# Kernel optimization log

Hardware: AMD Instinct MI355X
Metric: run time of the kernel (lower is better)

## Reference

```python
import jax, jax.numpy as jnp
import numpy as np

GROUP_SIZE = 128  # vLLM machete default group size
ZERO_POINT = 8.0  # uint4b8: stored unsigned 4-bit, logical value = q - 8


def setup_inputs() -> dict:
    key = jax.random.key(0)
    k_a, k_b, k_s = jax.random.split(key, 3)
    M, K, N = 4096, 4096, 12288
    a = jax.random.normal(k_a, (M, K), dtype=jnp.float32)
    # int4 quantized weights stored as small ints in [0, 16)
    b_q = jax.random.randint(k_b, (K, N), 0, 16, dtype=jnp.int32)
    # per-group scales: one scale per (group of 128 rows of K) per output column
    scales = jax.random.uniform(k_s, (K // GROUP_SIZE, N), dtype=jnp.float32) * 0.02 + 0.001
    return {"a": a, "b_q": b_q, "scales": scales}


def reference(a, b_q, scales):
    K, N = b_q.shape
    G = K // GROUP_SIZE
    # dequantize: (q - 8) * group_scale, scale broadcast over each K-group
    b = (b_q.astype(jnp.float32) - ZERO_POINT).reshape(G, GROUP_SIZE, N)
    b = (b * scales[:, None, :]).reshape(K, N)  # [K, N] dequantized weights
    return a @ b  # [M, N]
```

## Files before the change

kernel.cpp:

```cpp
#include <hip/hip_runtime.h>
#include <hip/hip_bf16.h>
#include <stdint.h>

constexpr int Mdim = 4096;
constexpr int Kdim = 4096;
constexpr int Ndim = 12288;

constexpr int NKT = Kdim / 64;
constexpr int GM256 = Mdim / 256;
constexpr int GN256 = Ndim / 256;
constexpr int NWG256 = GM256 * GN256;
constexpr int GRID_M = Mdim / 128;
constexpr int GRID_N = Ndim / 128;
constexpr int NWG = GRID_M * GRID_N;

typedef float  f32x4   __attribute__((ext_vector_type(4)));
typedef __bf16 bf16x4v __attribute__((ext_vector_type(4)));
typedef __bf16 bf16x8v __attribute__((ext_vector_type(8)));
typedef int    i32x4   __attribute__((ext_vector_type(4)));
typedef unsigned short ushort8 __attribute__((ext_vector_type(8)));

typedef __attribute__((address_space(3))) uint32_t       lds_u32;
typedef __attribute__((address_space(1))) const uint32_t glb_u32;

__device__ __forceinline__ void gload16(const void* g, void* l) {
    __builtin_amdgcn_global_load_lds((glb_u32*)(uintptr_t)g,
                                     (lds_u32*)(uint32_t)(uintptr_t)l, 16, 0, 0);
}


__launch_bounds__(256)
__global__ void cvtA(const float* __restrict__ A, unsigned short* __restrict__ Aw) {
    int t = blockIdx.x * 256 + threadIdx.x;
    int r = t >> 9;
    int c = t & 511;
    const float* src = A + ((long)r << 12) + (c << 3);
    f32x4 v0 = *(const f32x4*)src;
    f32x4 v1 = *(const f32x4*)(src + 4);
    bf16x8v o;
#pragma unroll
    for (int j = 0; j < 4; ++j) { o[j] = (__bf16)v0[j]; o[4 + j] = (__bf16)v1[j]; }
    int ks = c & 3;
    int cp = (c & ~3) | (ks ^ ((r >> 1) & 3));
    *(bf16x8v*)(Aw + ((long)r << 12) + (cp << 3)) = o;
}

__launch_bounds__(256)
__global__ void deqB(const int* __restrict__ Bq, const float* __restrict__ S,
                     unsigned short* __restrict__ Bw) {
    __shared__ unsigned short lt[64][72];
    int kb = blockIdx.x & 63;
    int nb = blockIdx.x >> 6;
    int k0 = kb << 6, n0 = nb << 6;
    int tid = threadIdx.x;
    int g = k0 >> 7;
    int nq = (tid & 15) << 2;
    f32x4 sc = *(const f32x4*)(S + (long)g * Ndim + n0 + nq);
#pragma unroll
    for (int p = 0; p < 4; ++p) {
        int kk = (p << 4) + (tid >> 4);
        i32x4 q = *(const i32x4*)(Bq + (long)(k0 + kk) * Ndim + n0 + nq);
#pragma unroll
        for (int j = 0; j < 4; ++j) {
            float v = ((float)q[j] - 8.f) * sc[j];
            lt[nq + j][kk] = __builtin_bit_cast(unsigned short, (__bf16)v);
        }
    }
    __syncthreads();
#pragma unroll
    for (int h = 0; h < 2; ++h) {
        int cidx = tid + (h << 8);
        int n = cidx >> 3, sidx = cidx & 7;
        int kh = sidx >> 2, ks = sidx & 3;
        int ksp = ks ^ ((n >> 1) & 3);
        ushort8 v = *(const ushort8*)&lt[n][sidx << 3];
        *(ushort8*)(Bw + (long)(n0 + n) * Kdim + k0 + kh * 32 + ksp * 8) = v;
    }
}

__launch_bounds__(512, 2)
__global__ void gemm256(const unsigned short* __restrict__ Aw,
                        const unsigned short* __restrict__ Bw,
                        float* __restrict__ C) {
    extern __shared__ unsigned char ldsbuf[];

    const int tid  = threadIdx.x;
    const int lane = tid & 63;
    const int w    = tid >> 6;
    const int wr   = w >> 2, wc = w & 3;
    const int fr   = lane & 15;
    const int ks   = lane >> 4;

    const int bid = blockIdx.x;
    const int xcd = bid & 7;
    const int loc = bid >> 3;
    const int pn  = loc >> 4;
    const int tm  = loc & 15;
    const int tn  = xcd * 6 + pn;
    const int brow = tm << 8, bcol = tn << 8;

    const unsigned char* pA = (const unsigned char*)Aw
        + (size_t)(brow + (tid >> 2)) * 8192 + (size_t)(tid & 3) * 16;
    const unsigned char* pA2 = pA + (size_t)128 * 8192;
    const unsigned char* pB = (const unsigned char*)Bw
        + (size_t)(bcol + (tid >> 2)) * 8192 + (size_t)(tid & 3) * 16;
    const unsigned char* pB2 = pB + (size_t)128 * 8192;
    const int ldw = w << 10;

    int offA[8][2], offB[4][2];
#pragma unroll
    for (int am = 0; am < 8; ++am)
#pragma unroll
        for (int kh = 0; kh < 2; ++kh) {
            int rowL = wr * 128 + am * 16 + fr;
            offA[am][kh] = (kh << 14) + rowL * 64 + ((ks ^ ((rowL >> 1) & 3)) << 4);
        }
#pragma unroll
    for (int n = 0; n < 4; ++n)
#pragma unroll
        for (int kh = 0; kh < 2; ++kh) {
            int colL = wc * 64 + n * 16 + fr;
            offB[n][kh] = (kh << 14) + colL * 64 + ((ks ^ ((colL >> 1) & 3)) << 4);
        }

    f32x4 acc[8][4];
#pragma unroll
    for (int m = 0; m < 8; ++m)
#pragma unroll
        for (int n = 0; n < 4; ++n) acc[m][n] = (f32x4){0.f, 0.f, 0.f, 0.f};

#define STG_A(DSTB, OFF)                                                      \
    gload16(pA  + (OFF), ldsbuf + (DSTB) + ldw);                              \
    gload16(pA2 + (OFF), ldsbuf + (DSTB) + ldw + 8192);
#define STG_B(DSTB, OFF)                                                      \
    gload16(pB  + (OFF), ldsbuf + (DSTB) + 32768 + ldw);                      \
    gload16(pB2 + (OFF), ldsbuf + (DSTB) + 32768 + ldw + 8192);

#define TILE(BUF, OFF, STG)                                                   \
    {                                                                         \
        unsigned char* sAc = ldsbuf + ((BUF) << 16);                          \
        unsigned char* sBc = sAc + 32768;                                     \
        bf16x8v a0[8], b0[4], a1[8], b1[4];                                   \
        _Pragma("unroll") for (int m = 0; m < 8; ++m)                         \
            a0[m] = *(const bf16x8v*)(sAc + offA[m][0]);                      \
        _Pragma("unroll") for (int n = 0; n < 4; ++n)                         \
            b0[n] = *(const bf16x8v*)(sBc + offB[n][0]);                      \
        if (STG) {                                                            \
            STG_A(((1 - (BUF)) << 16), OFF)                                   \
            STG_B(((1 - (BUF)) << 16), OFF)                                   \
            STG_A(((1 - (BUF)) << 16) + (1 << 14), (OFF) + 64)                \
            STG_B(((1 - (BUF)) << 16) + (1 << 14), (OFF) + 64)                \
        }                                                                     \
        __builtin_amdgcn_s_setprio(1);                                        \
        _Pragma("unroll") for (int m = 0; m < 8; ++m)                         \
            _Pragma("unroll") for (int n = 0; n < 4; ++n)                     \
                acc[m][n] = __builtin_amdgcn_mfma_f32_16x16x32_bf16(          \
                    a0[m], b0[n], acc[m][n], 0, 0, 0);                        \
        __builtin_amdgcn_s_setprio(0);                                        \
        _Pragma("unroll") for (int m = 0; m < 8; ++m)                         \
            a1[m] = *(const bf16x8v*)(sAc + offA[m][1]);                      \
        _Pragma("unroll") for (int n = 0; n < 4; ++n)                         \
            b1[n] = *(const bf16x8v*)(sBc + offB[n][1]);                      \
        __builtin_amdgcn_s_setprio(1);                                        \
        _Pragma("unroll") for (int m = 0; m < 8; ++m)                         \
            _Pragma("unroll") for (int n = 0; n < 4; ++n)                     \
                acc[m][n] = __builtin_amdgcn_mfma_f32_16x16x32_bf16(          \
                    a1[m], b1[n], acc[m][n], 0, 0, 0);                        \
        __builtin_amdgcn_s_setprio(0);                                        \
        asm volatile("s_waitcnt vmcnt(0)" ::: "memory");                      \
        __builtin_amdgcn_s_barrier();                                         \
    }

    STG_A(0, 0)          STG_B(0, 0)
    STG_A((1 << 14), 64) STG_B((1 << 14), 64)
    asm volatile("s_waitcnt vmcnt(0)" ::: "memory");
    __builtin_amdgcn_s_barrier();

    for (int it = 0; it < 31; ++it) {
        TILE(0, 128, 1)
        TILE(1, 256, 1)
        pA += 256; pA2 += 256; pB += 256; pB2 += 256;
    }
    TILE(0, 128, 1)
    TILE(1, 0, 0)

#pragma unroll
    for (int m = 0; m < 8; ++m) {
        int row = brow + wr * 128 + m * 16 + ks * 4;
#pragma unroll
        for (int n = 0; n < 4; ++n) {
            int col = bcol + wc * 64 + n * 16 + fr;
            f32x4 v = acc[m][n];
            float* cp = C + (size_t)row * Ndim + col;
#pragma unroll
            for (int r = 0; r < 4; ++r) cp[(size_t)r * Ndim] = v[r];
        }
    }
#undef TILE
#undef STG_B
#undef STG_A
}

__launch_bounds__(256, 3)
__global__ void gemm_bf16(const unsigned short* __restrict__ Aw,
                          const unsigned short* __restrict__ Bw,
                          float* __restrict__ C) {
    __shared__ unsigned char sA[128 * 64 * 2];
    __shared__ unsigned char sB[128 * 64 * 2];

    const int tid  = threadIdx.x;
    const int lane = tid & 63;
    const int w    = tid >> 6;

    const int bid   = blockIdx.x;
    const int x     = bid & 7;
    const int local = bid >> 3;
    const int pn    = local >> 5;
    const int tm    = local & 31;
    const int tn    = x * 12 + pn;
    const int brow  = tm << 7;
    const int bcol  = tn << 7;

    const unsigned char* ga[4];
    const unsigned char* gb[4];
#pragma unroll
    for (int i = 0; i < 4; ++i) {
        int c = (w << 8) + (i << 6) + lane;
        int r = c >> 3, s = c & 7;
        ga[i] = (const unsigned char*)Aw + (long)(brow + r) * 8192 + (s << 4);
        gb[i] = (const unsigned char*)Bw + (long)(bcol + r) * 8192 + (s << 4);
    }

    const int fr = lane & 15;
    const int ks = lane >> 4;
    const int wr = w >> 1, wc = w & 1;
    int ra[4][2], rb[4][2];
#pragma unroll
    for (int m = 0; m < 4; ++m)
#pragma unroll
        for (int kk = 0; kk < 2; ++kk) {
            int r_a = wr * 64 + m * 16 + fr;
            int r_b = wc * 64 + m * 16 + fr;
            ra[m][kk] = (r_a << 7) + (kk << 6) + ((ks ^ ((r_a >> 1) & 3)) << 4);
            rb[m][kk] = (r_b << 7) + (kk << 6) + ((ks ^ ((r_b >> 1) & 3)) << 4);
        }

    f32x4 acc[4][4];
#pragma unroll
    for (int m = 0; m < 4; ++m)
#pragma unroll
        for (int n = 0; n < 4; ++n) acc[m][n] = (f32x4){0.f, 0.f, 0.f, 0.f};

    for (int kt = 0; kt < NKT; ++kt) {
#pragma unroll
        for (int i = 0; i < 4; ++i) {
            gload16(ga[i], sA + (((w << 2) + i) << 10));
            gload16(gb[i], sB + (((w << 2) + i) << 10));
            ga[i] += 128;
            gb[i] += 128;
        }
        __syncthreads();

#pragma unroll
        for (int kk = 0; kk < 2; ++kk) {
            bf16x8v af[4], bf[4];
#pragma unroll
            for (int m = 0; m < 4; ++m) af[m] = *(const bf16x8v*)(sA + ra[m][kk]);
#pragma unroll
            for (int n = 0; n < 4; ++n) bf[n] = *(const bf16x8v*)(sB + rb[n][kk]);
#pragma unroll
            for (int m = 0; m < 4; ++m)
#pragma unroll
                for (int n = 0; n < 4; ++n)
                    acc[m][n] = __builtin_amdgcn_mfma_f32_16x16x32_bf16(af[m], bf[n], acc[m][n], 0, 0, 0);
        }
        __syncthreads();
    }

#pragma unroll
    for (int m = 0; m < 4; ++m) {
        int row = brow + wr * 64 + m * 16 + ks * 4;
#pragma unroll
        for (int n = 0; n < 4; ++n) {
            int col = bcol + wc * 64 + n * 16 + fr;
            f32x4 v = acc[m][n];
            float* cp = C + (long)row * Ndim + col;
#pragma unroll
            for (int r = 0; r < 4; ++r) cp[(long)r * Ndim] = v[r];
        }
    }
}

__device__ __forceinline__ int swz_f(int row, int kbyte) {
    int s = kbyte >> 4;
    int f = s ^ ((row ^ (row >> 2)) & 7);
    return (row << 7) + (f << 4) + (kbyte & 15);
}

__launch_bounds__(256, 2)
__global__ void machete_fused(const float* __restrict__ A,
                              const int* __restrict__ Bq,
                              const float* __restrict__ S,
                              float* __restrict__ C) {
    __shared__ unsigned char sA[128 * 64 * 2];
    __shared__ unsigned char sB[128 * 64 * 2];

    const int tid = threadIdx.x;
    const int bid = blockIdx.x;
    const int sid = (bid & 7) * (NWG / 8) + (bid >> 3);
    const int tm = sid / GRID_N;
    const int tn = sid % GRID_N;
    const int brow = tm * 128;
    const int bcol = tn * 128;

    const int a_row0 = tid >> 4;
    const int a_kb   = tid & 15;
    const int b_kb = tid >> 4;
    const int b_nb = tid & 15;

    int aw[8];
#pragma unroll
    for (int i = 0; i < 8; ++i) aw[i] = swz_f(a_row0 + 16 * i, a_kb * 8);
    int bw[2][4];
#pragma unroll
    for (int i = 0; i < 2; ++i)
#pragma unroll
        for (int j = 0; j < 4; ++j) bw[i][j] = swz_f(4 * b_nb + 64 * i + j, b_kb * 8);

    const int lane = tid & 63;
    const int w  = tid >> 6;
    const int wr = w >> 1, wc = w & 1;
    const int fr = lane & 15;
    const int ks = lane >> 4;
    int ar[4][2], br[4][2];
#pragma unroll
    for (int m = 0; m < 4; ++m)
#pragma unroll
        for (int kk = 0; kk < 2; ++kk) {
            ar[m][kk] = swz_f(wr * 64 + m * 16 + fr, kk * 64 + ks * 16);
            br[m][kk] = swz_f(wc * 64 + m * 16 + fr, kk * 64 + ks * 16);
        }

    const float* Ap = A + (long)brow * Kdim;
    const int*   Bp = Bq + bcol;

    f32x4 aregs[8];
    i32x4 bregs[2][4];
    f32x4 sregs[2];

#pragma unroll
    for (int i = 0; i < 8; ++i)
        aregs[i] = *(const f32x4*)(Ap + (long)(a_row0 + 16 * i) * Kdim + a_kb * 4);
#pragma unroll
    for (int i = 0; i < 2; ++i) {
#pragma unroll
        for (int r = 0; r < 4; ++r)
            bregs[i][r] = *(const i32x4*)(Bp + (long)(b_kb * 4 + r) * Ndim + 4 * b_nb + 64 * i);
        sregs[i] = *(const f32x4*)(S + bcol + 4 * b_nb + 64 * i);
    }

    f32x4 acc[4][4];
#pragma unroll
    for (int m = 0; m < 4; ++m)
#pragma unroll
        for (int n = 0; n < 4; ++n) acc[m][n] = (f32x4){0.f, 0.f, 0.f, 0.f};

    for (int kt = 0; kt < NKT; ++kt) {
#pragma unroll
        for (int i = 0; i < 8; ++i) {
            f32x4 v = aregs[i];
            bf16x4v p;
            p[0] = (__bf16)v[0]; p[1] = (__bf16)v[1];
            p[2] = (__bf16)v[2]; p[3] = (__bf16)v[3];
            *(bf16x4v*)(sA + aw[i]) = p;
        }
#pragma unroll
        for (int i = 0; i < 2; ++i) {
            f32x4 sc = sregs[i];
#pragma unroll
            for (int j = 0; j < 4; ++j) {
                float scj = sc[j];
                float nm8 = -8.f * scj;
                bf16x4v p;
#pragma unroll
                for (int r = 0; r < 4; ++r) {
                    float v = (float)bregs[i][r][j] * scj + nm8;
                    p[r] = (__bf16)v;
                }
                *(bf16x4v*)(sB + bw[i][j]) = p;
            }
        }
        __syncthreads();

        if (kt + 1 < NKT) {
            const float* Ap2 = Ap + (kt + 1) * 64;
            const int*   Bp2 = Bq + bcol + (long)((kt + 1) * 64) * Ndim;
            const float* Sp2 = S + (long)((kt + 1) >> 1) * Ndim + bcol;
#pragma unroll
            for (int i = 0; i < 8; ++i)
                aregs[i] = *(const f32x4*)(Ap2 + (long)(a_row0 + 16 * i) * Kdim + a_kb * 4);
#pragma unroll
            for (int i = 0; i < 2; ++i) {
#pragma unroll
                for (int r = 0; r < 4; ++r)
                    bregs[i][r] = *(const i32x4*)(Bp2 + (long)(b_kb * 4 + r) * Ndim + 4 * b_nb + 64 * i);
                sregs[i] = *(const f32x4*)(Sp2 + 4 * b_nb + 64 * i);
            }
        }

#pragma unroll
        for (int kk = 0; kk < 2; ++kk) {
            bf16x8v af[4], bfv[4];
#pragma unroll
            for (int m = 0; m < 4; ++m) af[m] = *(const bf16x8v*)(sA + ar[m][kk]);
#pragma unroll
            for (int n = 0; n < 4; ++n) bfv[n] = *(const bf16x8v*)(sB + br[n][kk]);
#pragma unroll
            for (int m = 0; m < 4; ++m)
#pragma unroll
                for (int n = 0; n < 4; ++n)
                    acc[m][n] = __builtin_amdgcn_mfma_f32_16x16x32_bf16(af[m], bfv[n], acc[m][n], 0, 0, 0);
        }
        __syncthreads();
    }

#pragma unroll
    for (int m = 0; m < 4; ++m) {
        int row = brow + wr * 64 + m * 16 + ks * 4;
#pragma unroll
        for (int n = 0; n < 4; ++n) {
            int col = bcol + wc * 64 + n * 16 + fr;
            f32x4 v = acc[m][n];
            float* cp = C + (long)row * Ndim + col;
#pragma unroll
            for (int r = 0; r < 4; ++r) cp[(long)r * Ndim] = v[r];
        }
    }
}

extern "C" void kernel_launch(void* const* d_in, const int* in_sizes, int n_in,
                              void* d_out, int out_size, void* d_ws, size_t ws_size,
                              hipStream_t stream) {
    const float* A  = (const float*)d_in[0];
    const int*   Bq = (const int*)d_in[1];
    const float* S  = (const float*)d_in[2];
    float* C = (float*)d_out;

    const size_t a_elems = (size_t)Mdim * Kdim;
    const size_t b_elems = (size_t)Ndim * Kdim;
    const size_t need = (a_elems + b_elems) * sizeof(unsigned short);

    if (ws_size >= need) {
        unsigned short* Aw = (unsigned short*)d_ws;
        unsigned short* Bw = Aw + a_elems;
        hipLaunchKernelGGL(cvtA, dim3((Mdim * Kdim / 8) / 256), dim3(256), 0, stream, A, Aw);
        hipLaunchKernelGGL(deqB, dim3((Kdim / 64) * (Ndim / 64)), dim3(256), 0, stream, Bq, S, Bw);
        hipError_t e = hipFuncSetAttribute(
            reinterpret_cast<const void*>(gemm256),
            hipFuncAttributeMaxDynamicSharedMemorySize, 131072);
        if (e == hipSuccess) {
            hipLaunchKernelGGL(gemm256, dim3(NWG256), dim3(512), 131072, stream, Aw, Bw, C);
        } else {
            hipLaunchKernelGGL(gemm_bf16, dim3(NWG), dim3(256), 0, stream, Aw, Bw, C);
        }
    } else {
        hipLaunchKernelGGL(machete_fused, dim3(NWG), dim3(256), 0, stream, A, Bq, S, C);
    }
}
```

Measured before the change: 477.7 us.

## Split each K-tile into four barrier-synchronized phases with partial vmcnt waits

Each double-buffered tile is split into four phases, each covering half the N fragments and half of K. Every phase issues one slice of the global-to-LDS staging loads and then runs a 16-MFMA block between barriers. The full vmcnt(0) drain at the end of each tile becomes vmcnt(4), which lets the latest loads stay in flight while earlier halves of the buffer are consumed. The aim is to interleave memory traffic with matrix math more finely, at the cost of more barriers per tile and fewer fragments held per phase.

```diff
diff --git a/kernel.cpp b/kernel.cpp
--- a/kernel.cpp
+++ b/kernel.cpp
@@ -136,53 +136,50 @@
     gload16(pB  + (OFF), ldsbuf + (DSTB) + 32768 + ldw);                      \
     gload16(pB2 + (OFF), ldsbuf + (DSTB) + 32768 + ldw + 8192);
 
-#define TILE(BUF, OFF, STG)                                                   \
+#define PHASE(SAc, SBc, NH, KH, DO_STG, STG_STMT, VM)                         \
+    {                                                                         \
+        bf16x8v aF[8], bF[2];                                                 \
+        _Pragma("unroll") for (int mf = 0; mf < 8; ++mf)                      \
+            aF[mf] = *(const bf16x8v*)((SAc) + offA[mf][KH]);                 \
+        _Pragma("unroll") for (int nf = 0; nf < 2; ++nf)                      \
+            bF[nf] = *(const bf16x8v*)((SBc) + offB[(NH) * 2 + nf][KH]);      \
+        if (DO_STG) { STG_STMT }                                              \
+        __builtin_amdgcn_s_barrier();                                         \
+        __builtin_amdgcn_s_setprio(1);                                        \
+        _Pragma("unroll") for (int mf = 0; mf < 8; ++mf)                      \
+            _Pragma("unroll") for (int nf = 0; nf < 2; ++nf)                  \
+                acc[mf][(NH) * 2 + nf] =                                      \
+                    __builtin_amdgcn_mfma_f32_16x16x32_bf16(                  \
+                        aF[mf], bF[nf], acc[mf][(NH) * 2 + nf], 0, 0, 0);     \
+        __builtin_amdgcn_s_setprio(0);                                        \
+        if ((VM) == 4)      asm volatile("s_waitcnt vmcnt(4)" ::: "memory");  \
+        else if ((VM) == 0) asm volatile("s_waitcnt vmcnt(0)" ::: "memory");  \
+        __builtin_amdgcn_s_barrier();                                         \
+    }
+
+#define TILE(BUF, OFF, STG, VM2, VM4)                                         \
     {                                                                         \
         unsigned char* sAc = ldsbuf + ((BUF) << 16);                          \
         unsigned char* sBc = sAc + 32768;                                     \
-        bf16x8v a0[8], b0[4], a1[8], b1[4];                                   \
-        _Pragma("unroll") for (int m = 0; m < 8; ++m)                         \
-            a0[m] = *(const bf16x8v*)(sAc + offA[m][0]);                      \
-        _Pragma("unroll") for (int n = 0; n < 4; ++n)                         \
-            b0[n] = *(const bf16x8v*)(sBc + offB[n][0]);                      \
-        if (STG) {                                                            \
-            STG_A(((1 - (BUF)) << 16), OFF)                                   \
-            STG_B(((1 - (BUF)) << 16), OFF)                                   \
-            STG_A(((1 - (BUF)) << 16) + (1 << 14), (OFF) + 64)                \
-            STG_B(((1 - (BUF)) << 16) + (1 << 14), (OFF) + 64)                \
-        }                                                                     \
-        __builtin_amdgcn_s_setprio(1);                                        \
-        _Pragma("unroll") for (int m = 0; m < 8; ++m)                         \
-            _Pragma("unroll") for (int n = 0; n < 4; ++n)                     \
-                acc[m][n] = __builtin_amdgcn_mfma_f32_16x16x32_bf16(          \
-                    a0[m], b0[n], acc[m][n], 0, 0, 0);                        \
-        __builtin_amdgcn_s_setprio(0);                                        \
-        _Pragma("unroll") for (int m = 0; m < 8; ++m)                         \
-            a1[m] = *(const bf16x8v*)(sAc + offA[m][1]);                      \
-        _Pragma("unroll") for (int n = 0; n < 4; ++n)                         \
-            b1[n] = *(const bf16x8v*)(sBc + offB[n][1]);                      \
-        __builtin_amdgcn_s_setprio(1);                                        \
-        _Pragma("unroll") for (int m = 0; m < 8; ++m)                         \
-            _Pragma("unroll") for (int n = 0; n < 4; ++n)                     \
-                acc[m][n] = __builtin_amdgcn_mfma_f32_16x16x32_bf16(          \
-                    a1[m], b1[n], acc[m][n], 0, 0, 0);                        \
-        __builtin_amdgcn_s_setprio(0);                                        \
-        asm volatile("s_waitcnt vmcnt(0)" ::: "memory");                      \
-        __builtin_amdgcn_s_barrier();                                         \
+        const int ob = (1 - (BUF)) << 16;                                     \
+        PHASE(sAc, sBc, 0, 0, STG, STG_A(ob, OFF), -1)                        \
+        PHASE(sAc, sBc, 1, 0, STG, STG_B(ob, OFF), VM2)                       \
+        PHASE(sAc, sBc, 0, 1, STG, STG_A(ob + (1 << 14), (OFF) + 64), -1)     \
+        PHASE(sAc, sBc, 1, 1, STG, STG_B(ob + (1 << 14), (OFF) + 64), VM4)    \
     }
 
     STG_A(0, 0)          STG_B(0, 0)
     STG_A((1 << 14), 64) STG_B((1 << 14), 64)
-    asm volatile("s_waitcnt vmcnt(0)" ::: "memory");
+    asm volatile("s_waitcnt vmcnt(4)" ::: "memory");
     __builtin_amdgcn_s_barrier();
 
     for (int it = 0; it < 31; ++it) {
-        TILE(0, 128, 1)
-        TILE(1, 256, 1)
+        TILE(0, 128, 1, 4, 4)
+        TILE(1, 256, 1, 4, 4)
         pA += 256; pA2 += 256; pB += 256; pB2 += 256;
     }
-    TILE(0, 128, 1)
-    TILE(1, 0, 0)
+    TILE(0, 128, 1, 4, 4)
+    TILE(1, 0, 0, 0, -1)
 
 #pragma unroll
     for (int m = 0; m < 8; ++m) {
@@ -197,6 +194,7 @@
         }
     }
 #undef TILE
+#undef PHASE
 #undef STG_B
 #undef STG_A
 }
```

Result: no change. 482.0 us (+0.9%).

## Load A fragments directly from global into registers, stage only B in LDS

Applied to the files above, without the earlier changes.

The 256x256 GEMM stops staging A tiles through LDS. Each wave now loads its A MFMA fragments straight from global memory into registers, one k-step ahead (double-buffered registers aK0/aK1), while B stays double-buffered in LDS. The A-side XOR swizzle is removed from cvtA and from the fallback kernel to match. This halves LDS use (64KB) and removes A LDS reads, at the cost of more register pressure, uncoalesced 16-byte global loads per lane, and partial vmcnt waits that rely on load ordering.

```diff
diff --git a/kernel.cpp b/kernel.cpp
--- a/kernel.cpp
+++ b/kernel.cpp
@@ -27,7 +27,6 @@
     __builtin_amdgcn_global_load_lds((glb_u32*)(uintptr_t)g,
                                      (lds_u32*)(uint32_t)(uintptr_t)l, 16, 0, 0);
 }
-
 
 __launch_bounds__(256)
 __global__ void cvtA(const float* __restrict__ A, unsigned short* __restrict__ Aw) {
@@ -40,9 +39,7 @@
     bf16x8v o;
 #pragma unroll
     for (int j = 0; j < 4; ++j) { o[j] = (__bf16)v0[j]; o[4 + j] = (__bf16)v1[j]; }
-    int ks = c & 3;
-    int cp = (c & ~3) | (ks ^ ((r >> 1) & 3));
-    *(bf16x8v*)(Aw + ((long)r << 12) + (cp << 3)) = o;
+    *(bf16x8v*)(Aw + ((long)r << 12) + (c << 3)) = o;
 }
 
 __launch_bounds__(256)
@@ -82,7 +79,7 @@
 __global__ void gemm256(const unsigned short* __restrict__ Aw,
                         const unsigned short* __restrict__ Bw,
                         float* __restrict__ C) {
-    extern __shared__ unsigned char ldsbuf[];
+    extern __shared__ unsigned char ldsb[];
 
     const int tid  = threadIdx.x;
     const int lane = tid & 63;
@@ -99,22 +96,15 @@
     const int tn  = xcd * 6 + pn;
     const int brow = tm << 8, bcol = tn << 8;
 
-    const unsigned char* pA = (const unsigned char*)Aw
-        + (size_t)(brow + (tid >> 2)) * 8192 + (size_t)(tid & 3) * 16;
-    const unsigned char* pA2 = pA + (size_t)128 * 8192;
     const unsigned char* pB = (const unsigned char*)Bw
         + (size_t)(bcol + (tid >> 2)) * 8192 + (size_t)(tid & 3) * 16;
     const unsigned char* pB2 = pB + (size_t)128 * 8192;
     const int ldw = w << 10;
 
-    int offA[8][2], offB[4][2];
-#pragma unroll
-    for (int am = 0; am < 8; ++am)
-#pragma unroll
-        for (int kh = 0; kh < 2; ++kh) {
-            int rowL = wr * 128 + am * 16 + fr;
-            offA[am][kh] = (kh << 14) + rowL * 64 + ((ks ^ ((rowL >> 1) & 3)) << 4);
-        }
+    const unsigned char* aP = (const unsigned char*)Aw
+        + (size_t)(brow + wr * 128 + fr) * 8192 + (size_t)ks * 16;
+
+    int offB[4][2];
 #pragma unroll
     for (int n = 0; n < 4; ++n)
 #pragma unroll
@@ -129,57 +119,61 @@
 #pragma unroll
         for (int n = 0; n < 4; ++n) acc[m][n] = (f32x4){0.f, 0.f, 0.f, 0.f};
 
-#define STG_A(DSTB, OFF)                                                      \
-    gload16(pA  + (OFF), ldsbuf + (DSTB) + ldw);                              \
-    gload16(pA2 + (OFF), ldsbuf + (DSTB) + ldw + 8192);
-#define STG_B(DSTB, OFF)                                                      \
-    gload16(pB  + (OFF), ldsbuf + (DSTB) + 32768 + ldw);                      \
-    gload16(pB2 + (OFF), ldsbuf + (DSTB) + 32768 + ldw + 8192);
+    bf16x8v aK0[8], aK1[8];
+
+#define STG_B(BUFB, OFF)                                                      \
+    gload16(pB  + (OFF),      ldsb + (BUFB) + ldw);                           \
+    gload16(pB2 + (OFF),      ldsb + (BUFB) + ldw + 8192);                    \
+    gload16(pB  + (OFF) + 64, ldsb + (BUFB) + 16384 + ldw);                   \
+    gload16(pB2 + (OFF) + 64, ldsb + (BUFB) + 16384 + ldw + 8192);
+
+#define LOAD_A(dst, OFF)                                                      \
+    _Pragma("unroll") for (int mf = 0; mf < 8; ++mf)                          \
+        dst[mf] = *(const bf16x8v*)(aP + (size_t)mf * 131072 + (OFF));
+
+#define MFMA32(Aset, Bset)                                                    \
+    _Pragma("unroll") for (int mf = 0; mf < 8; ++mf)                          \
+        _Pragma("unroll") for (int nf = 0; nf < 4; ++nf)                      \
+            acc[mf][nf] = __builtin_amdgcn_mfma_f32_16x16x32_bf16(            \
+                (Aset)[mf], (Bset)[nf], acc[mf][nf], 0, 0, 0);
 
 #define TILE(BUF, OFF, STG)                                                   \
     {                                                                         \
-        unsigned char* sAc = ldsbuf + ((BUF) << 16);                          \
-        unsigned char* sBc = sAc + 32768;                                     \
-        bf16x8v a0[8], b0[4], a1[8], b1[4];                                   \
-        _Pragma("unroll") for (int m = 0; m < 8; ++m)                         \
-            a0[m] = *(const bf16x8v*)(sAc + offA[m][0]);                      \
-        _Pragma("unroll") for (int n = 0; n < 4; ++n)                         \
-            b0[n] = *(const bf16x8v*)(sBc + offB[n][0]);                      \
+        unsigned char* bufc = ldsb + (BUF) * 32768;                           \
+        bf16x8v b0[4], b1[4];                                                 \
+        _Pragma("unroll") for (int nf = 0; nf < 4; ++nf)                      \
+            b0[nf] = *(const bf16x8v*)(bufc + offB[nf][0]);                   \
         if (STG) {                                                            \
-            STG_A(((1 - (BUF)) << 16), OFF)                                   \
-            STG_B(((1 - (BUF)) << 16), OFF)                                   \
-            STG_A(((1 - (BUF)) << 16) + (1 << 14), (OFF) + 64)                \
-            STG_B(((1 - (BUF)) << 16) + (1 << 14), (OFF) + 64)                \
+            STG_B((1 - (BUF)) * 32768, OFF)                                   \
+            asm volatile("" ::: "memory");   \
         }                                                                     \
         __builtin_amdgcn_s_setprio(1);                                        \
-        _Pragma("unroll") for (int m = 0; m < 8; ++m)                         \
-            _Pragma("unroll") for (int n = 0; n < 4; ++n)                     \
-                acc[m][n] = __builtin_amdgcn_mfma_f32_16x16x32_bf16(          \
-                    a0[m], b0[n], acc[m][n], 0, 0, 0);                        \
+        MFMA32(aK0, b0)                                                       \
         __builtin_amdgcn_s_setprio(0);                                        \
-        _Pragma("unroll") for (int m = 0; m < 8; ++m)                         \
-            a1[m] = *(const bf16x8v*)(sAc + offA[m][1]);                      \
-        _Pragma("unroll") for (int n = 0; n < 4; ++n)                         \
-            b1[n] = *(const bf16x8v*)(sBc + offB[n][1]);                      \
+        _Pragma("unroll") for (int nf = 0; nf < 4; ++nf)                      \
+            b1[nf] = *(const bf16x8v*)(bufc + offB[nf][1]);                   \
+        if (STG) { LOAD_A(aK0, OFF) }                                         \
         __builtin_amdgcn_s_setprio(1);                                        \
-        _Pragma("unroll") for (int m = 0; m < 8; ++m)                         \
-            _Pragma("unroll") for (int n = 0; n < 4; ++n)                     \
-                acc[m][n] = __builtin_amdgcn_mfma_f32_16x16x32_bf16(          \
-                    a1[m], b1[n], acc[m][n], 0, 0, 0);                        \
+        MFMA32(aK1, b1)                                                       \
         __builtin_amdgcn_s_setprio(0);                                        \
-        asm volatile("s_waitcnt vmcnt(0)" ::: "memory");                      \
-        __builtin_amdgcn_s_barrier();                                         \
-    }
-
-    STG_A(0, 0)          STG_B(0, 0)
-    STG_A((1 << 14), 64) STG_B((1 << 14), 64)
-    asm volatile("s_waitcnt vmcnt(0)" ::: "memory");
+        if (STG) {                                                            \
+            LOAD_A(aK1, (OFF) + 64)                                           \
+            asm volatile("s_waitcnt vmcnt(16)" ::: "memory");                 \
+            __builtin_amdgcn_s_barrier();                                     \
+        }                                                                     \
+    }
+
+    STG_B(0, 0)
+    asm volatile("" ::: "memory");
+    LOAD_A(aK0, 0)
+    LOAD_A(aK1, 64)
+    asm volatile("s_waitcnt vmcnt(16)" ::: "memory");
     __builtin_amdgcn_s_barrier();
 
     for (int it = 0; it < 31; ++it) {
         TILE(0, 128, 1)
         TILE(1, 256, 1)
-        pA += 256; pA2 += 256; pB += 256; pB2 += 256;
+        pB += 256; pB2 += 256; aP += 256;
     }
     TILE(0, 128, 1)
     TILE(1, 0, 0)
@@ -197,8 +191,9 @@
         }
     }
 #undef TILE
+#undef MFMA32
+#undef LOAD_A
 #undef STG_B
-#undef STG_A
 }
 
 __launch_bounds__(256, 3)
@@ -241,7 +236,7 @@
         for (int kk = 0; kk < 2; ++kk) {
             int r_a = wr * 64 + m * 16 + fr;
             int r_b = wc * 64 + m * 16 + fr;
-            ra[m][kk] = (r_a << 7) + (kk << 6) + ((ks ^ ((r_a >> 1) & 3)) << 4);
+            ra[m][kk] = (r_a << 7) + (kk << 6) + (ks << 4);
             rb[m][kk] = (r_b << 7) + (kk << 6) + ((ks ^ ((r_b >> 1) & 3)) << 4);
         }
 
@@ -457,9 +452,9 @@
         hipLaunchKernelGGL(deqB, dim3((Kdim / 64) * (Ndim / 64)), dim3(256), 0, stream, Bq, S, Bw);
         hipError_t e = hipFuncSetAttribute(
             reinterpret_cast<const void*>(gemm256),
-            hipFuncAttributeMaxDynamicSharedMemorySize, 131072);
+            hipFuncAttributeMaxDynamicSharedMemorySize, 65536);
         if (e == hipSuccess) {
-            hipLaunchKernelGGL(gemm256, dim3(NWG256), dim3(512), 131072, stream, Aw, Bw, C);
+            hipLaunchKernelGGL(gemm256, dim3(NWG256), dim3(512), 65536, stream, Aw, Bw, C);
         } else {
             hipLaunchKernelGGL(gemm_bf16, dim3(NWG), dim3(256), 0, stream, Aw, Bw, C);
         }
```

Result: slower. 1.110 ms (+132.3%).
